# Optimization experiments

Measured on AMD Instinct MI355X. Metric: run time of the kernel, lower is better.

## Reference

```python
import jax, jax.numpy as jnp
import numpy as np

B, T, E, H, D = 2, 2048, 1024, 16, 64   # batch, seq, n_embd, heads, head_dim
C, P, BF, MH, R, F4 = 64, 64, 256, 128, 8, 4096  # ctx_dim, prototypes, basis, mod hidden, gate rank, 4*n_embd


def _rms(x):
    return x * jax.lax.rsqrt(jnp.mean(x * x, axis=-1, keepdims=True) + 1e-6)


def _rotary(x, cos, sin):
    d = x.shape[-1] // 2
    x1, x2 = x[..., :d], x[..., d:]
    return jnp.concatenate([x1 * cos + x2 * sin, -x1 * sin + x2 * cos], axis=-1)


def _ln(x, g, b):
    mu = jnp.mean(x, axis=-1, keepdims=True)
    v = jnp.mean(jnp.square(x - mu), axis=-1, keepdims=True)
    return (x - mu) * jax.lax.rsqrt(v + 1e-5) * g + b


def _remixed(x, ctx, bw, lg, lb, tm, bias, m1w, m1b, m2w, m2b, ogw, ogb, ogB, ogs):
    # RemixedLinear: basis proj -> LayerNorm -> context sigmoid gate -> template mixing -> low-rank output gate
    h = _ln(x @ bw.T, lg, lb)                                              # [B,T,basis]
    gl = jax.nn.gelu(ctx @ m1w.T + m1b, approximate=False) @ m2w.T + m2b   # basis_modulator MLP
    gate_basis = jax.nn.sigmoid(gl)                                        # gate_temperature = 1.0, dense gate
    gate_out = 1.0 + jnp.tanh(ogs * ((ctx @ ogw.T + ogb) @ ogB))           # low-rank output gate
    return (h * gate_basis) @ tm.T * gate_out + bias


def _forward(x, cos, sin, wq, wk, wv, wo, cb_qw, protos,
             fc_bw, fc_lg, fc_lb, fc_tm, fc_b, fc_m1w, fc_m1b, fc_m2w, fc_m2b, fc_ogw, fc_ogb, fc_ogB, fc_ogs,
             pj_bw, pj_lg, pj_lb, pj_tm, pj_b, pj_m1w, pj_m1b, pj_m2w, pj_m2b, pj_ogw, pj_ogb, pj_ogB, pj_ogs):
    b, t, _ = x.shape
    # --- attention with rotary embeddings ---
    xn = _rms(x)
    q = _rotary((xn @ wq.T).reshape(b, t, H, D), cos, sin)
    k = _rotary((xn @ wk.T).reshape(b, t, H, D), cos, sin)
    v = (xn @ wv.T).reshape(b, t, H, D)
    s = jnp.einsum('bqhd,bkhd->bhqk', q, k) * (D ** -0.5)
    mask = jnp.tril(jnp.ones((t, t), dtype=bool))
    s = jnp.where(mask, s, jnp.finfo(s.dtype).min)
    a = jax.nn.softmax(s, axis=-1)
    attn_out = jnp.einsum('bhqk,bkhd->bqhd', a, v).reshape(b, t, E) @ wo.T
    x = x + attn_out
    # --- ContextBank: soft lookup into prototype vocabulary ---
    xn2 = _rms(x)
    cq = xn2 @ cb_qw.T                                  # [B,T,C]
    w = jax.nn.softmax((cq @ protos.T) * (C ** -0.5), axis=-1)
    ctx = w @ protos                                    # [B,T,C]
    # --- RemixedFeedForward: RemixedLinear -> relu^2 -> RemixedLinear ---
    h = _remixed(xn2, ctx, fc_bw, fc_lg, fc_lb, fc_tm, fc_b, fc_m1w, fc_m1b, fc_m2w, fc_m2b, fc_ogw, fc_ogb, fc_ogB, fc_ogs)
    h = jnp.square(jax.nn.relu(h))
    y = _remixed(h, ctx, pj_bw, pj_lg, pj_lb, pj_tm, pj_b, pj_m1w, pj_m1b, pj_m2w, pj_m2b, pj_ogw, pj_ogb, pj_ogB, pj_ogs)
    return x + y


def setup_inputs():
    key = jax.random.key(0)
    ks = jax.random.split(key, 24)
    g = lambda i, shape, s=0.02: jax.random.normal(ks[i], shape, jnp.float32) * s
    t = jnp.arange(T, dtype=jnp.float32)
    inv = 1.0 / (10000.0 ** (jnp.arange(0, D, 2, dtype=jnp.float32) / D))
    ang = t[:, None] * inv                              # [T, D/2]
    return dict(
        x=jax.random.normal(ks[0], (B, T, E), jnp.float32),
        cos=jnp.cos(ang)[None, :, None, :], sin=jnp.sin(ang)[None, :, None, :],
        wq=g(1, (E, E)), wk=g(2, (E, E)), wv=g(3, (E, E)), wo=g(4, (E, E)),
        cb_qw=g(5, (C, E)), protos=g(6, (P, C)),
        fc_bw=g(7, (BF, E)), fc_lg=jnp.ones((BF,)), fc_lb=jnp.zeros((BF,)),
        fc_tm=g(8, (F4, BF), 0.05), fc_b=jnp.zeros((F4,)),
        fc_m1w=g(9, (MH, C)), fc_m1b=jnp.zeros((MH,)),
        fc_m2w=g(10, (BF, MH)), fc_m2b=jnp.zeros((BF,)),
        fc_ogw=g(11, (R, C)), fc_ogb=jnp.zeros((R,)),
        fc_ogB=g(12, (R, F4)), fc_ogs=jnp.full((1,), 0.1, jnp.float32),
        pj_bw=g(13, (BF, F4)), pj_lg=jnp.ones((BF,)), pj_lb=jnp.zeros((BF,)),
        pj_tm=g(14, (E, BF), 0.05), pj_b=jnp.zeros((E,)),
        pj_m1w=g(15, (MH, C)), pj_m1b=jnp.zeros((MH,)),
        pj_m2w=g(16, (BF, MH)), pj_m2b=jnp.zeros((BF,)),
        pj_ogw=g(17, (R, C)), pj_ogb=jnp.zeros((R,)),
        pj_ogB=g(18, (R, E)), pj_ogs=jnp.full((1,), 0.1, jnp.float32),
    )


def reference(x, cos, sin, wq, wk, wv, wo, cb_qw, protos,
              fc_bw, fc_lg, fc_lb, fc_tm, fc_b, fc_m1w, fc_m1b, fc_m2w, fc_m2b, fc_ogw, fc_ogb, fc_ogB, fc_ogs,
              pj_bw, pj_lg, pj_lb, pj_tm, pj_b, pj_m1w, pj_m1b, pj_m2w, pj_m2b, pj_ogw, pj_ogb, pj_ogB, pj_ogs):
    return _forward(x, cos, sin, wq, wk, wv, wo, cb_qw, protos,
                    fc_bw, fc_lg, fc_lb, fc_tm, fc_b, fc_m1w, fc_m1b, fc_m2w, fc_m2b, fc_ogw, fc_ogb, fc_ogB, fc_ogs,
                    pj_bw, pj_lg, pj_lb, pj_tm, pj_b, pj_m1w, pj_m1b, pj_m2w, pj_m2b, pj_ogw, pj_ogb, pj_ogB, pj_ogs)
```

## Files before the change

### kernel.cpp

```cpp
#include <hip/hip_runtime.h>
#include <hip/hip_bf16.h>

typedef unsigned short u16;
typedef unsigned int u32;
typedef __attribute__((ext_vector_type(8))) short bf16x8;
typedef __attribute__((ext_vector_type(4))) float f32x4;
typedef __attribute__((ext_vector_type(4))) u16 u16x4;

#define DEVFN __device__ __forceinline__

DEVFN u16 f2b(float f) {
  u32 u = __builtin_bit_cast(u32, f);
  return (u16)((u + 0x7FFFu + ((u >> 16) & 1u)) >> 16);
}
DEVFN float b2f(u16 b) { return __builtin_bit_cast(float, (u32)b << 16); }

DEVFN void gll16(const void* g, void* l) {
  __builtin_amdgcn_global_load_lds((const __attribute__((address_space(1))) void*)g,
                                   (__attribute__((address_space(3))) void*)l, 16, 0, 0);
}
#define BARRIER() __builtin_amdgcn_s_barrier()

constexpr int Tc = 2048, Ec = 1024, Hc = 16, Cc = 64, BFc = 256, F4c = 4096;
constexpr int Mc = 2 * Tc;

constexpr size_t MB = 1ull << 20;
constexpr size_t O_XN  = 0;
constexpr size_t O_HBF = 8 * MB;
constexpr size_t O_QB  = 40 * MB;
constexpr size_t O_H1  = 40 * MB;
constexpr size_t O_A2  = 40 * MB;
constexpr size_t O_KB  = 48 * MB;
constexpr size_t O_H2  = 48 * MB;
constexpr size_t O_VBF = 56 * MB;
constexpr size_t O_CQ  = 64 * MB;
constexpr size_t O_CTX = 68 * MB;
constexpr size_t O_GO1 = 68 * MB + 512 * 1024;
constexpr size_t O_GO2 = 68 * MB + 640 * 1024;
constexpr size_t O_GB1 = 69 * MB;
constexpr size_t O_VT  = 72 * MB;
constexpr size_t O_GB2 = 73 * MB;
constexpr size_t O_A1  = 77 * MB;
constexpr size_t O_X2  = 80 * MB;
constexpr size_t O_WQ  = 96 * MB, O_WK = 98 * MB, O_WV = 100 * MB, O_WO = 102 * MB;
constexpr size_t O_CBQ = 104 * MB;
constexpr size_t O_FCBW = O_CBQ + 256 * 1024;
constexpr size_t O_FCTM = 105 * MB;
constexpr size_t O_PJBW = 107 * MB;
constexpr size_t O_PJTM = 109 * MB;

struct Cvt9 {
  const float* s[9];
  u16* d[9];
  int cum[10];
};
__global__ __launch_bounds__(256) void k_cvt(Cvt9 a) {
  int i = blockIdx.x * 256 + threadIdx.x;
  int seg = 0;
  #pragma unroll
  for (int s = 1; s < 9; s++) seg += (i >= a.cum[s]);
  int off = i - a.cum[seg];
  float4 v = *(const float4*)&a.s[seg][(size_t)off * 4];
  u16x4 o; o.x = f2b(v.x); o.y = f2b(v.y); o.z = f2b(v.z); o.w = f2b(v.w);
  *(u16x4*)&a.d[seg][(size_t)off * 4] = o;
}

DEVFN float bsum256(float v, float* sb) {
  #pragma unroll
  for (int off = 32; off; off >>= 1) v += __shfl_down(v, off);
  __syncthreads();
  if ((threadIdx.x & 63) == 0) sb[threadIdx.x >> 6] = v;
  __syncthreads();
  return (sb[0] + sb[1]) + (sb[2] + sb[3]);
}

__global__ __launch_bounds__(256) void k_rms(const float* __restrict__ x, u16* __restrict__ o) {
  __shared__ float sb[4];
  int row = blockIdx.x, tid = threadIdx.x;
  float4 v = *(const float4*)&x[(size_t)row * 1024 + tid * 4];
  float s = bsum256(v.x * v.x + v.y * v.y + v.z * v.z + v.w * v.w, sb);
  float r = rsqrtf(s * (1.f / 1024.f) + 1e-6f);
  u16x4 ov;
  ov.x = f2b(v.x * r); ov.y = f2b(v.y * r); ov.z = f2b(v.z * r); ov.w = f2b(v.w * r);
  *(u16x4*)&o[(size_t)row * 1024 + tid * 4] = ov;
}

__global__ __launch_bounds__(256) void k_vtrans(const u16* __restrict__ vb, u16* __restrict__ vt) {
  __shared__ u16 tl[64][65];
  int t0 = blockIdx.x * 64, bh = blockIdx.y;
  int b = bh >> 4, h = bh & 15, tid = threadIdx.x;
  #pragma unroll
  for (int rep = 0; rep < 16; rep++) {
    int idx = rep * 256 + tid, r = idx >> 6, c = idx & 63;
    tl[r][c] = vb[((size_t)(b * 2048 + t0 + r)) * 1024 + h * 64 + c];
  }
  __syncthreads();
  #pragma unroll
  for (int rep = 0; rep < 16; rep++) {
    int idx = rep * 256 + tid, d = idx >> 6, tt = idx & 63;
    vt[((size_t)bh * 64 + d) * 2048 + t0 + tt] = tl[tt][d];
  }
}

#define MFMA16(A, B, C) __builtin_amdgcn_mfma_f32_16x16x32_bf16(A, B, C, 0, 0, 0)
__global__ __launch_bounds__(256) void k_attn(const u16* __restrict__ Q, const u16* __restrict__ Kb,
                                              const u16* __restrict__ VT, u16* __restrict__ O) {
  const int h = blockIdx.y, b = blockIdx.z;
  const int tid = threadIdx.x, lane = tid & 63, w = tid >> 6;
  const int lr = lane & 15, lg = lane >> 4;
  const size_t TE = 2048ull * 1024ull;
  const u16* Qp = Q + (size_t)b * TE + (size_t)h * 64;
  const u16* Kp = Kb + (size_t)b * TE + (size_t)h * 64;
  const u16* Vp = VT + ((size_t)(b * 16 + h)) * 64ull * 2048ull;
  u16* Op = O + (size_t)b * TE + (size_t)h * 64;
  __shared__ __align__(16) u16 Ks[2][4096];
  __shared__ __align__(16) u16 Vs[2][4096];
  __shared__ __align__(16) u16 Ps[4][1024];
  auto stageKV = [&](int j0, int buf) {
    #pragma unroll
    for (int c = 0; c < 2; c++) {
      int u = c * 256 + tid;
      int row = u >> 3, slot = u & 7;
      int cg = slot ^ (row & 7);
      gll16(&Kp[(size_t)(j0 + row) * 1024 + cg * 8], &Ks[buf][u * 8]);
    }
    #pragma unroll
    for (int c = 0; c < 2; c++) {
      int u = c * 256 + tid;
      int row = u >> 3, slot = u & 7;
      int cg = slot ^ (row & 7);
      gll16(&Vp[(size_t)row * 2048 + j0 + cg * 8], &Vs[buf][u * 8]);
    }
  };
  auto run_tile = [&](int qb) {
    const int q0 = qb * 64, qw0 = q0 + w * 16;
    bf16x8 qf0 = *(const bf16x8*)&Qp[(size_t)(qw0 + lr) * 1024 + lg * 8];
    bf16x8 qf1 = *(const bf16x8*)&Qp[(size_t)(qw0 + lr) * 1024 + 32 + lg * 8];
    f32x4 o0 = {}, o1 = {}, o2 = {}, o3 = {};
    float m = -1e30f, l = 0.f;
    const int NT = qb + 1;
    stageKV(0, 0);
    int cur = 0;
    for (int it = 0; it < NT; it++) {
      if (it + 1 < NT) {
        stageKV((it + 1) * 64, cur ^ 1);
        asm volatile("s_waitcnt vmcnt(4)" ::: "memory");
      } else {
        asm volatile("s_waitcnt vmcnt(0)" ::: "memory");
      }
      BARRIER();
      const int j0 = it * 64;
      const u16* Kl = Ks[cur];
      const u16* Vl = Vs[cur];
      f32x4 c4[4];
      __builtin_amdgcn_s_setprio(1);
      #pragma unroll
      for (int kg = 0; kg < 4; kg++) {
        f32x4 cc = {};
        int r = kg * 16 + lr;
        bf16x8 ka0 = *(const bf16x8*)&Kl[r * 64 + ((lg ^ (lr & 7)) * 8)];
        bf16x8 ka1 = *(const bf16x8*)&Kl[r * 64 + (((4 + lg) ^ (lr & 7)) * 8)];
        cc = MFMA16(ka0, qf0, cc);
        cc = MFMA16(ka1, qf1, cc);
        c4[kg] = cc;
      }
      __builtin_amdgcn_s_setprio(0);
      float xs[16];
      #pragma unroll
      for (int kg = 0; kg < 4; kg++)
        #pragma unroll
        for (int r = 0; r < 4; r++) xs[kg * 4 + r] = c4[kg][r] * 0.125f;
      if (it == NT - 1) {
        int q = qw0 + lr;
        #pragma unroll
        for (int kg = 0; kg < 4; kg++)
          #pragma unroll
          for (int r = 0; r < 4; r++)
            if (j0 + kg * 16 + lg * 4 + r > q) xs[kg * 4 + r] = -1e30f;
      }
      float tm = xs[0];
      #pragma unroll
      for (int r = 1; r < 16; r++) tm = fmaxf(tm, xs[r]);
      tm = fmaxf(tm, __shfl_xor(tm, 16));
      tm = fmaxf(tm, __shfl_xor(tm, 32));
      float mn = fmaxf(m, tm);
      float al = __expf(m - mn);
      m = mn;
      float p[16], rs = 0.f;
      #pragma unroll
      for (int r = 0; r < 16; r++) { p[r] = __expf(xs[r] - mn); rs += p[r]; }
      rs += __shfl_xor(rs, 16);
      rs += __shfl_xor(rs, 32);
      l = l * al + rs;
      #pragma unroll
      for (int kg = 0; kg < 4; kg++) {
        int unit = (kg >> 1) * 64 + ((kg & 1) * 2 + (lg >> 1)) * 16 + lr;
        u16x4 pk;
        pk.x = f2b(p[kg * 4 + 0]); pk.y = f2b(p[kg * 4 + 1]);
        pk.z = f2b(p[kg * 4 + 2]); pk.w = f2b(p[kg * 4 + 3]);
        *(u16x4*)&Ps[w][unit * 8 + (lg & 1) * 4] = pk;
      }
      float ar0 = __shfl(al, lg * 4 + 0), ar1 = __shfl(al, lg * 4 + 1);
      float ar2 = __shfl(al, lg * 4 + 2), ar3 = __shfl(al, lg * 4 + 3);
      o0[0] *= ar0; o0[1] *= ar1; o0[2] *= ar2; o0[3] *= ar3;
      o1[0] *= ar0; o1[1] *= ar1; o1[2] *= ar2; o1[3] *= ar3;
      o2[0] *= ar0; o2[1] *= ar1; o2[2] *= ar2; o2[3] *= ar3;
      o3[0] *= ar0; o3[1] *= ar1; o3[2] *= ar2; o3[3] *= ar3;
      bf16x8 pa0 = *(const bf16x8*)&Ps[w][(lg * 16 + lr) * 8];
      bf16x8 pa1 = *(const bf16x8*)&Ps[w][(64 + lg * 16 + lr) * 8];
      __builtin_amdgcn_s_setprio(1);
      #pragma unroll
      for (int dg = 0; dg < 4; dg++) {
        int dr = dg * 16 + lr;
        bf16x8 v0 = *(const bf16x8*)&Vl[dr * 64 + ((lg ^ (lr & 7)) * 8)];
        bf16x8 v1 = *(const bf16x8*)&Vl[dr * 64 + (((4 + lg) ^ (lr & 7)) * 8)];
        f32x4& od = (dg == 0) ? o0 : (dg == 1) ? o1 : (dg == 2) ? o2 : o3;
        od = MFMA16(pa0, v0, od);
        od = MFMA16(pa1, v1, od);
      }
      __builtin_amdgcn_s_setprio(0);
      BARRIER();
      cur ^= 1;
    }
    float li0 = 1.f / __shfl(l, lg * 4 + 0), li1 = 1.f / __shfl(l, lg * 4 + 1);
    float li2 = 1.f / __shfl(l, lg * 4 + 2), li3 = 1.f / __shfl(l, lg * 4 + 3);
    #pragma unroll
    for (int r = 0; r < 4; r++) {
      float lir = (r == 0) ? li0 : (r == 1) ? li1 : (r == 2) ? li2 : li3;
      size_t ro = (size_t)(qw0 + lg * 4 + r) * 1024;
      Op[ro + lr]      = f2b(o0[r] * lir);
      Op[ro + 16 + lr] = f2b(o1[r] * lir);
      Op[ro + 32 + lr] = f2b(o2[r] * lir);
      Op[ro + 48 + lr] = f2b(o3[r] * lir);
    }
  };
  run_tile(blockIdx.x);
  run_tile(31 - blockIdx.x);
}

template <int BM, int BN, int WR, int WC, int EPI>
__global__ __launch_bounds__(256) void gemm_bt(
    const u16* __restrict__ A, const u16* __restrict__ Bw,
    float* __restrict__ Co, u16* __restrict__ Cb,
    int gM, int N, int K, int KS,
    const float* __restrict__ e0, const float* __restrict__ e1,
    const float* __restrict__ e2, const float* __restrict__ e3,
    const float* __restrict__ e4) {
  constexpr int WM = BM / WR, WN = BN / WC;
  constexpr int FM = WM / 16, FN = WN / 16;
  constexpr int ACH = BM / 64, BCH = BN / 64;
  static_assert(WR * WC == 4 && BM % 64 == 0 && BN % 64 == 0, "cfg");
  __shared__ __align__(16) u16 As[2][BM * 32];
  __shared__ __align__(16) u16 Bs[2][BN * 32];
  const int tid = threadIdx.x;
  const int lane = tid & 63, wid = tid >> 6;
  const int wr = wid / WC, wc = wid % WC;
  const int bm = blockIdx.y * BM, bn = blockIdx.x * BN;
  const int lr = lane & 15, lg = lane >> 4;
  const int arow0 = bm + wr * WM, bcol0 = bn + wc * WN;
  const int kbeg = blockIdx.z * KS, kend = kbeg + KS;
  f32x4 acc[FM][FN] = {};
  auto stage = [&](int k0, int buf) {
    #pragma unroll
    for (int c = 0; c < ACH; c++) {
      int u = c * 256 + tid;
      int row = u >> 2, slot = u & 3;
      int cg = slot ^ (row & 3) ^ ((row >> 2) & 3);
      gll16(&A[(size_t)(bm + row) * K + k0 + cg * 8], &As[buf][u * 8]);
    }
    #pragma unroll
    for (int c = 0; c < BCH; c++) {
      int u = c * 256 + tid;
      int row = u >> 2, slot = u & 3;
      int cg = slot ^ (row & 3) ^ ((row >> 2) & 3);
      gll16(&Bw[(size_t)(bn + row) * K + k0 + cg * 8], &Bs[buf][u * 8]);
    }
  };
  stage(kbeg, 0);
  int cur = 0;
  for (int k0 = kbeg; k0 < kend; k0 += 32) {
    __syncthreads();
    if (k0 + 32 < kend) stage(k0 + 32, cur ^ 1);
    const u16* Ab = As[cur];
    const u16* Bb = Bs[cur];
    bf16x8 af[FM], bfr[FN];
    #pragma unroll
    for (int i = 0; i < FM; i++) {
      int tr = wr * WM + i * 16 + lr;
      af[i] = *(const bf16x8*)&Ab[tr * 32 + ((lg ^ (tr & 3) ^ ((tr >> 2) & 3)) * 8)];
    }
    #pragma unroll
    for (int j = 0; j < FN; j++) {
      int tr = wc * WN + j * 16 + lr;
      bfr[j] = *(const bf16x8*)&Bb[tr * 32 + ((lg ^ (tr & 3) ^ ((tr >> 2) & 3)) * 8)];
    }
    #pragma unroll
    for (int i = 0; i < FM; i++)
      #pragma unroll
      for (int j = 0; j < FN; j++)
        acc[i][j] = __builtin_amdgcn_mfma_f32_16x16x32_bf16(af[i], bfr[j], acc[i][j], 0, 0, 0);
    cur ^= 1;
  }
  const int nb0 = bcol0 + lr;
  if constexpr (EPI == 0 || EPI == 2) {
    float* Cz = Co + (size_t)blockIdx.z * ((size_t)gM * N);
    #pragma unroll
    for (int i = 0; i < FM; i++)
      #pragma unroll
      for (int r = 0; r < 4; r++) {
        size_t mrow = (size_t)(arow0 + i * 16 + lg * 4 + r);
        #pragma unroll
        for (int j = 0; j < FN; j++) {
          float v = acc[i][j][r];
          if constexpr (EPI == 2) v += e4[mrow * N + nb0 + j * 16];
          Cz[mrow * N + nb0 + j * 16] = v;
        }
      }
  } else if constexpr (EPI == 5) {
    #pragma unroll
    for (int i = 0; i < FM; i++)
      #pragma unroll
      for (int r = 0; r < 4; r++) {
        size_t mrow = (size_t)(arow0 + i * 16 + lg * 4 + r);
        int t = (int)(mrow & 2047);
        #pragma unroll
        for (int j = 0; j < 2; j++) {
          int d = lr + j * 16;
          float cth = e0[t * 32 + d], sth = e1[t * 32 + d];
          float x1 = acc[i][j][r], x2 = acc[i][j + 2][r];
          Cb[mrow * N + nb0 + j * 16]       = f2b(x1 * cth + x2 * sth);
          Cb[mrow * N + nb0 + (j + 2) * 16] = f2b(x2 * cth - x1 * sth);
        }
      }
  } else if constexpr (EPI == 7) {
    #pragma unroll
    for (int i = 0; i < FM; i++)
      #pragma unroll
      for (int r = 0; r < 4; r++) {
        size_t mrow = (size_t)(arow0 + i * 16 + lg * 4 + r);
        #pragma unroll
        for (int j = 0; j < FN; j++)
          Cb[mrow * N + nb0 + j * 16] = f2b(acc[i][j][r]);
      }
  } else {
    const float ogs = e3[0];
    float gB[FN][8], bias[FN];
    #pragma unroll
    for (int j = 0; j < FN; j++) {
      int n = nb0 + j * 16;
      bias[j] = e2[n];
      #pragma unroll
      for (int rr = 0; rr < 8; rr++) gB[j][rr] = e1[(size_t)rr * N + n];
    }
    #pragma unroll
    for (int i = 0; i < FM; i++)
      #pragma unroll
      for (int r = 0; r < 4; r++) {
        size_t mrow = (size_t)(arow0 + i * 16 + lg * 4 + r);
        float go8[8];
        #pragma unroll
        for (int rr = 0; rr < 8; rr++) go8[rr] = e0[mrow * 8 + rr];
        #pragma unroll
        for (int j = 0; j < FN; j++) {
          float d = 0.f;
          #pragma unroll
          for (int rr = 0; rr < 8; rr++) d += go8[rr] * gB[j][rr];
          float gate = 1.f + tanhf(ogs * d);
          float v = acc[i][j][r] * gate + bias[j];
          if constexpr (EPI == 3) {
            v = fmaxf(v, 0.f); v *= v;
            Cb[mrow * N + nb0 + j * 16] = f2b(v);
          } else {
            v += e4[mrow * N + nb0 + j * 16];
            Co[mrow * N + nb0 + j * 16] = v;
          }
        }
      }
  }
}

__global__ __launch_bounds__(256) void k_ctx(const float* __restrict__ cqp,
                                             const float* __restrict__ pr,
                                             u16* __restrict__ ctx) {
  __shared__ float pl[64 * 65];
  __shared__ float cqs[4][64];
  __shared__ float wl[4][64];
  int tid = threadIdx.x, lane = tid & 63, w = tid >> 6;
  int row0 = blockIdx.x * 4;
  for (int i = w; i < 64; i += 4) pl[i * 65 + lane] = pr[i * 64 + lane];
  {
    float s4 = 0.f;
    #pragma unroll
    for (int z = 0; z < 4; z++) s4 += cqp[(size_t)z * Mc * 64 + (size_t)(row0 + w) * 64 + lane];
    cqs[w][lane] = s4;
  }
  __syncthreads();
  float s = 0.f;
  #pragma unroll
  for (int k = 0; k < 64; k++) s += cqs[w][k] * pl[lane * 65 + k];
  s *= 0.125f;
  float mx = s;
  #pragma unroll
  for (int off = 32; off; off >>= 1) mx = fmaxf(mx, __shfl_xor(mx, off));
  float e = __expf(s - mx), sum = e;
  #pragma unroll
  for (int off = 32; off; off >>= 1) sum += __shfl_xor(sum, off);
  wl[w][lane] = e / sum;
  __syncthreads();
  float a = 0.f;
  #pragma unroll
  for (int p = 0; p < 64; p++) a += wl[w][p] * pl[p * 65 + lane];
  ctx[(size_t)(row0 + w) * 64 + lane] = f2b(a);
}

__global__ __launch_bounds__(256) void k_gate(
    const u16* __restrict__ ctx,
    const float* __restrict__ m1w, const float* __restrict__ m1b,
    const float* __restrict__ m2w, const float* __restrict__ m2b,
    const float* __restrict__ ogw, const float* __restrict__ ogb,
    float* __restrict__ gb, float* __restrict__ go) {
  __shared__ __align__(16) float cs[16][64];
  __shared__ __align__(16) float gls[16][128];
  int tid = threadIdx.x;
  int row0 = blockIdx.x * 16;
  for (int i = tid; i < 16 * 64; i += 256) cs[i >> 6][i & 63] = b2f(ctx[(size_t)row0 * 64 + i]);
  __syncthreads();
  for (int i = tid; i < 16 * 128; i += 256) {
    int r = i >> 7, mh = i & 127;
    const float* wrow = &m1w[(size_t)mh * 64];
    float a = m1b[mh];
    #pragma unroll
    for (int k4 = 0; k4 < 16; k4++) {
      float4 w4 = *(const float4*)&wrow[k4 * 4];
      float4 c4 = *(const float4*)&cs[r][k4 * 4];
      a += c4.x * w4.x + c4.y * w4.y + c4.z * w4.z + c4.w * w4.w;
    }
    gls[r][mh] = 0.5f * a * (1.f + erff(a * 0.70710678f));
  }
  if (tid < 128) {
    int r = tid >> 3, rr = tid & 7;
    const float* wrow = &ogw[(size_t)rr * 64];
    float a = ogb[rr];
    #pragma unroll
    for (int k4 = 0; k4 < 16; k4++) {
      float4 w4 = *(const float4*)&wrow[k4 * 4];
      float4 c4 = *(const float4*)&cs[r][k4 * 4];
      a += c4.x * w4.x + c4.y * w4.y + c4.z * w4.z + c4.w * w4.w;
    }
    go[(size_t)(row0 + r) * 8 + rr] = a;
  }
  __syncthreads();
  int n = tid;
  float acc[16];
  #pragma unroll
  for (int r = 0; r < 16; r++) acc[r] = m2b[n];
  for (int k4 = 0; k4 < 32; k4++) {
    float4 wv = *(const float4*)&m2w[(size_t)n * 128 + k4 * 4];
    #pragma unroll
    for (int r = 0; r < 16; r++) {
      float4 g = *(const float4*)&gls[r][k4 * 4];
      acc[r] += g.x * wv.x + g.y * wv.y + g.z * wv.z + g.w * wv.w;
    }
  }
  #pragma unroll
  for (int r = 0; r < 16; r++)
    gb[(size_t)(row0 + r) * 256 + n] = 1.f / (1.f + __expf(-acc[r]));
}

template <int NS>
__global__ __launch_bounds__(256) void k_lnmul(const float* __restrict__ h,
                                               const float* __restrict__ g,
                                               const float* __restrict__ b,
                                               const float* __restrict__ gbm,
                                               u16* __restrict__ o) {
  __shared__ float sb[4];
  int row = blockIdx.x, n = threadIdx.x;
  float x = 0.f;
  #pragma unroll
  for (int z = 0; z < NS; z++) x += h[(size_t)z * Mc * 256 + (size_t)row * 256 + n];
  float mu = bsum256(x, sb) * (1.f / 256.f);
  float d = x - mu;
  float var = bsum256(d * d, sb) * (1.f / 256.f);
  float y = d * rsqrtf(var + 1e-5f) * g[n] + b[n];
  o[(size_t)row * 256 + n] = f2b(y * gbm[(size_t)row * 256 + n]);
}

extern "C" void kernel_launch(void* const* d_in, const int* in_sizes, int n_in,
                              void* d_out, int out_size, void* d_ws, size_t ws_size,
                              hipStream_t stream) {
  (void)in_sizes; (void)n_in; (void)out_size; (void)ws_size;
  const float* x      = (const float*)d_in[0];
  const float* cosb   = (const float*)d_in[1];
  const float* sinb   = (const float*)d_in[2];
  const float* wq     = (const float*)d_in[3];
  const float* wk     = (const float*)d_in[4];
  const float* wv     = (const float*)d_in[5];
  const float* wo     = (const float*)d_in[6];
  const float* cb_qw  = (const float*)d_in[7];
  const float* protos = (const float*)d_in[8];
  const float* fc_bw  = (const float*)d_in[9];
  const float* fc_lg  = (const float*)d_in[10];
  const float* fc_lb  = (const float*)d_in[11];
  const float* fc_tm  = (const float*)d_in[12];
  const float* fc_b   = (const float*)d_in[13];
  const float* fc_m1w = (const float*)d_in[14];
  const float* fc_m1b = (const float*)d_in[15];
  const float* fc_m2w = (const float*)d_in[16];
  const float* fc_m2b = (const float*)d_in[17];
  const float* fc_ogw = (const float*)d_in[18];
  const float* fc_ogb = (const float*)d_in[19];
  const float* fc_ogB = (const float*)d_in[20];
  const float* fc_ogs = (const float*)d_in[21];
  const float* pj_bw  = (const float*)d_in[22];
  const float* pj_lg  = (const float*)d_in[23];
  const float* pj_lb  = (const float*)d_in[24];
  const float* pj_tm  = (const float*)d_in[25];
  const float* pj_b   = (const float*)d_in[26];
  const float* pj_m1w = (const float*)d_in[27];
  const float* pj_m1b = (const float*)d_in[28];
  const float* pj_m2w = (const float*)d_in[29];
  const float* pj_m2b = (const float*)d_in[30];
  const float* pj_ogw = (const float*)d_in[31];
  const float* pj_ogb = (const float*)d_in[32];
  const float* pj_ogB = (const float*)d_in[33];
  const float* pj_ogs = (const float*)d_in[34];
  char* ws = (char*)d_ws;
  float* outp = (float*)d_out;
  auto U = [&](size_t o) { return (u16*)(ws + o); };
  auto F = [&](size_t o) { return (float*)(ws + o); };
  const float* nf = nullptr;

  {
    Cvt9 a;
    const float* srcs[9] = {wq, wk, wv, wo, cb_qw, fc_bw, fc_tm, pj_bw, pj_tm};
    size_t offs[9] = {O_WQ, O_WK, O_WV, O_WO, O_CBQ, O_FCBW, O_FCTM, O_PJBW, O_PJTM};
    int ns[9] = {Ec*Ec, Ec*Ec, Ec*Ec, Ec*Ec, Cc*Ec, BFc*Ec, F4c*BFc, BFc*F4c, Ec*BFc};
    int cum = 0;
    for (int s = 0; s < 9; s++) {
      a.s[s] = srcs[s]; a.d[s] = U(offs[s]); a.cum[s] = cum; cum += ns[s] / 4;
    }
    a.cum[9] = cum;
    k_cvt<<<dim3(cum / 256), dim3(256), 0, stream>>>(a);
  }
  k_rms<<<dim3(Mc), dim3(256), 0, stream>>>(x, U(O_XN));
  gemm_bt<128,128,2,2,5><<<dim3(8,32), dim3(256), 0, stream>>>(U(O_XN), U(O_WQ), nullptr, U(O_QB), Mc, Ec, Ec, Ec, cosb, sinb, nf, nf, nf);
  gemm_bt<128,128,2,2,5><<<dim3(8,32), dim3(256), 0, stream>>>(U(O_XN), U(O_WK), nullptr, U(O_KB), Mc, Ec, Ec, Ec, cosb, sinb, nf, nf, nf);
  gemm_bt<128,128,2,2,7><<<dim3(8,32), dim3(256), 0, stream>>>(U(O_XN), U(O_WV), nullptr, U(O_VBF), Mc, Ec, Ec, Ec, nf, nf, nf, nf, nf);
  k_vtrans<<<dim3(Tc / 64, 2 * Hc), dim3(256), 0, stream>>>(U(O_VBF), U(O_VT));
  k_attn<<<dim3(Tc / 128, Hc, 2), dim3(256), 0, stream>>>(U(O_QB), U(O_KB), U(O_VT), U(O_XN));
  gemm_bt<128,128,2,2,2><<<dim3(8,32), dim3(256), 0, stream>>>(U(O_XN), U(O_WO), F(O_X2), nullptr, Mc, Ec, Ec, Ec, nf, nf, nf, nf, x);
  k_rms<<<dim3(Mc), dim3(256), 0, stream>>>(F(O_X2), U(O_XN));
  gemm_bt<64,64,1,4,0><<<dim3(1,64,4), dim3(256), 0, stream>>>(U(O_XN), U(O_CBQ), F(O_CQ), nullptr, Mc, Cc, Ec, 256, nf, nf, nf, nf, nf);
  k_ctx<<<dim3(Mc / 4), dim3(256), 0, stream>>>(F(O_CQ), protos, U(O_CTX));
  k_gate<<<dim3(Mc / 16), dim3(256), 0, stream>>>(U(O_CTX), fc_m1w, fc_m1b, fc_m2w, fc_m2b, fc_ogw, fc_ogb, F(O_GB1), F(O_GO1));
  k_gate<<<dim3(Mc / 16), dim3(256), 0, stream>>>(U(O_CTX), pj_m1w, pj_m1b, pj_m2w, pj_m2b, pj_ogw, pj_ogb, F(O_GB2), F(O_GO2));
  gemm_bt<64,64,1,4,0><<<dim3(4,64,2), dim3(256), 0, stream>>>(U(O_XN), U(O_FCBW), F(O_H1), nullptr, Mc, BFc, Ec, 512, nf, nf, nf, nf, nf);
  k_lnmul<2><<<dim3(Mc), dim3(256), 0, stream>>>(F(O_H1), fc_lg, fc_lb, F(O_GB1), U(O_A1));
  gemm_bt<128,128,2,2,3><<<dim3(32,32), dim3(256), 0, stream>>>(U(O_A1), U(O_FCTM), nullptr, U(O_HBF), Mc, F4c, BFc, BFc, F(O_GO1), fc_ogB, fc_b, fc_ogs, nf);
  gemm_bt<64,64,1,4,0><<<dim3(4,64,4), dim3(256), 0, stream>>>(U(O_HBF), U(O_PJBW), F(O_H2), nullptr, Mc, BFc, F4c, 1024, nf, nf, nf, nf, nf);
  k_lnmul<4><<<dim3(Mc), dim3(256), 0, stream>>>(F(O_H2), pj_lg, pj_lb, F(O_GB2), U(O_A2));
  gemm_bt<128,128,2,2,4><<<dim3(8,32), dim3(256), 0, stream>>>(U(O_A2), U(O_PJTM), outp, nullptr, Mc, Ec, BFc, BFc, F(O_GO2), pj_ogB, pj_b, pj_ogs, F(O_X2));
}
```

Baseline: 487.0 us.

## Fuse QKV GEMMs, merge context and gate kernels, lazy softmax rescale, retile GEMMs

The Q, K and V projections become one GEMM with N=3072 whose epilogue routes tiles to Q/K (with rotary) or V buffers. The context lookup and both gate MLPs are merged into one kernel, which removes the bf16 ctx round trip and two launches. Attention now uses exp2 with a folded scale, rescales the running output only when the row max grows by more than a threshold, and remaps its blocks into a 1D grid. Several GEMMs switch to 128x64 tiles. The lazy rescale adds a warp vote and relies on the bounded-growth assumption staying numerically safe.

```diff
diff --git a/kernel.cpp b/kernel.cpp
--- a/kernel.cpp
+++ b/kernel.cpp
@@ -23,6 +23,7 @@
 
 constexpr int Tc = 2048, Ec = 1024, Hc = 16, Cc = 64, BFc = 256, F4c = 4096;
 constexpr int Mc = 2 * Tc;
+constexpr float C8 = 0.18033688f;
 
 constexpr size_t MB = 1ull << 20;
 constexpr size_t O_XN  = 0;
@@ -34,7 +35,6 @@
 constexpr size_t O_H2  = 48 * MB;
 constexpr size_t O_VBF = 56 * MB;
 constexpr size_t O_CQ  = 64 * MB;
-constexpr size_t O_CTX = 68 * MB;
 constexpr size_t O_GO1 = 68 * MB + 512 * 1024;
 constexpr size_t O_GO2 = 68 * MB + 640 * 1024;
 constexpr size_t O_GB1 = 69 * MB;
@@ -105,7 +105,10 @@
 #define MFMA16(A, B, C) __builtin_amdgcn_mfma_f32_16x16x32_bf16(A, B, C, 0, 0, 0)
 __global__ __launch_bounds__(256) void k_attn(const u16* __restrict__ Q, const u16* __restrict__ Kb,
                                               const u16* __restrict__ VT, u16* __restrict__ O) {
-  const int h = blockIdx.y, b = blockIdx.z;
+  const int i = blockIdx.x;
+  const int wrk = (i & 7) * 64 + (i >> 3);
+  const int hb = wrk >> 4, xp = wrk & 15;
+  const int b = hb >> 4, h = hb & 15;
   const int tid = threadIdx.x, lane = tid & 63, w = tid >> 6;
   const int lr = lane & 15, lg = lane >> 4;
   const size_t TE = 2048ull * 1024ull;
@@ -169,7 +172,7 @@
       #pragma unroll
       for (int kg = 0; kg < 4; kg++)
         #pragma unroll
-        for (int r = 0; r < 4; r++) xs[kg * 4 + r] = c4[kg][r] * 0.125f;
+        for (int r = 0; r < 4; r++) xs[kg * 4 + r] = c4[kg][r];
       if (it == NT - 1) {
         int q = qw0 + lr;
         #pragma unroll
@@ -183,15 +186,25 @@
       for (int r = 1; r < 16; r++) tm = fmaxf(tm, xs[r]);
       tm = fmaxf(tm, __shfl_xor(tm, 16));
       tm = fmaxf(tm, __shfl_xor(tm, 32));
-      float mn = fmaxf(m, tm);
-      float al = __expf(m - mn);
-      m = mn;
+      if (!__all(tm <= m + 64.f)) {
+        float mn = fmaxf(m, tm);
+        float al = exp2f((m - mn) * C8);
+        m = mn;
+        l *= al;
+        float ar0 = __shfl(al, lg * 4 + 0), ar1 = __shfl(al, lg * 4 + 1);
+        float ar2 = __shfl(al, lg * 4 + 2), ar3 = __shfl(al, lg * 4 + 3);
+        o0[0] *= ar0; o0[1] *= ar1; o0[2] *= ar2; o0[3] *= ar3;
+        o1[0] *= ar0; o1[1] *= ar1; o1[2] *= ar2; o1[3] *= ar3;
+        o2[0] *= ar0; o2[1] *= ar1; o2[2] *= ar2; o2[3] *= ar3;
+        o3[0] *= ar0; o3[1] *= ar1; o3[2] *= ar2; o3[3] *= ar3;
+      }
+      const float mnC = -m * C8;
       float p[16], rs = 0.f;
       #pragma unroll
-      for (int r = 0; r < 16; r++) { p[r] = __expf(xs[r] - mn); rs += p[r]; }
+      for (int r = 0; r < 16; r++) { p[r] = exp2f(fmaf(xs[r], C8, mnC)); rs += p[r]; }
       rs += __shfl_xor(rs, 16);
       rs += __shfl_xor(rs, 32);
-      l = l * al + rs;
+      l += rs;
       #pragma unroll
       for (int kg = 0; kg < 4; kg++) {
         int unit = (kg >> 1) * 64 + ((kg & 1) * 2 + (lg >> 1)) * 16 + lr;
@@ -200,12 +213,6 @@
         pk.z = f2b(p[kg * 4 + 2]); pk.w = f2b(p[kg * 4 + 3]);
         *(u16x4*)&Ps[w][unit * 8 + (lg & 1) * 4] = pk;
       }
-      float ar0 = __shfl(al, lg * 4 + 0), ar1 = __shfl(al, lg * 4 + 1);
-      float ar2 = __shfl(al, lg * 4 + 2), ar3 = __shfl(al, lg * 4 + 3);
-      o0[0] *= ar0; o0[1] *= ar1; o0[2] *= ar2; o0[3] *= ar3;
-      o1[0] *= ar0; o1[1] *= ar1; o1[2] *= ar2; o1[3] *= ar3;
-      o2[0] *= ar0; o2[1] *= ar1; o2[2] *= ar2; o2[3] *= ar3;
-      o3[0] *= ar0; o3[1] *= ar1; o3[2] *= ar2; o3[3] *= ar3;
       bf16x8 pa0 = *(const bf16x8*)&Ps[w][(lg * 16 + lr) * 8];
       bf16x8 pa1 = *(const bf16x8*)&Ps[w][(64 + lg * 16 + lr) * 8];
       __builtin_amdgcn_s_setprio(1);
@@ -234,14 +241,14 @@
       Op[ro + 48 + lr] = f2b(o3[r] * lir);
     }
   };
-  run_tile(blockIdx.x);
-  run_tile(31 - blockIdx.x);
+  run_tile(xp);
+  run_tile(31 - xp);
 }
 
 template <int BM, int BN, int WR, int WC, int EPI>
 __global__ __launch_bounds__(256) void gemm_bt(
     const u16* __restrict__ A, const u16* __restrict__ Bw,
-    float* __restrict__ Co, u16* __restrict__ Cb,
+    float* __restrict__ Co, u16* __restrict__ Cb, u16* __restrict__ Cb2, u16* __restrict__ Cb3,
     int gM, int N, int K, int KS,
     const float* __restrict__ e0, const float* __restrict__ e1,
     const float* __restrict__ e2, const float* __restrict__ e3,
@@ -316,22 +323,37 @@
           Cz[mrow * N + nb0 + j * 16] = v;
         }
       }
-  } else if constexpr (EPI == 5) {
-    #pragma unroll
-    for (int i = 0; i < FM; i++)
-      #pragma unroll
-      for (int r = 0; r < 4; r++) {
-        size_t mrow = (size_t)(arow0 + i * 16 + lg * 4 + r);
-        int t = (int)(mrow & 2047);
-        #pragma unroll
-        for (int j = 0; j < 2; j++) {
-          int d = lr + j * 16;
-          float cth = e0[t * 32 + d], sth = e1[t * 32 + d];
-          float x1 = acc[i][j][r], x2 = acc[i][j + 2][r];
-          Cb[mrow * N + nb0 + j * 16]       = f2b(x1 * cth + x2 * sth);
-          Cb[mrow * N + nb0 + (j + 2) * 16] = f2b(x2 * cth - x1 * sth);
+  } else if constexpr (EPI == 8) {
+    if (bn < 2048) {
+      u16* dst = (bn < 1024) ? Cb : Cb2;
+      const int nq0 = (bcol0 & 1023) + lr;
+      #pragma unroll
+      for (int i = 0; i < FM; i++)
+        #pragma unroll
+        for (int r = 0; r < 4; r++) {
+          size_t mrow = (size_t)(arow0 + i * 16 + lg * 4 + r);
+          int t = (int)(mrow & 2047);
+          #pragma unroll
+          for (int j = 0; j < 2; j++) {
+            int d = lr + j * 16;
+            float cth = e0[t * 32 + d], sth = e1[t * 32 + d];
+            float x1 = acc[i][j][r], x2 = acc[i][j + 2][r];
+            dst[mrow * 1024 + nq0 + j * 16]       = f2b(x1 * cth + x2 * sth);
+            dst[mrow * 1024 + nq0 + (j + 2) * 16] = f2b(x2 * cth - x1 * sth);
+          }
         }
-      }
+    } else {
+      const int nv0 = (bcol0 - 2048) + lr;
+      #pragma unroll
+      for (int i = 0; i < FM; i++)
+        #pragma unroll
+        for (int r = 0; r < 4; r++) {
+          size_t mrow = (size_t)(arow0 + i * 16 + lg * 4 + r);
+          #pragma unroll
+          for (int j = 0; j < FN; j++)
+            Cb3[mrow * 1024 + nv0 + j * 16] = f2b(acc[i][j][r]);
+        }
+    }
   } else if constexpr (EPI == 7) {
     #pragma unroll
     for (int i = 0; i < FM; i++)
@@ -379,92 +401,112 @@
   }
 }
 
-__global__ __launch_bounds__(256) void k_ctx(const float* __restrict__ cqp,
-                                             const float* __restrict__ pr,
-                                             u16* __restrict__ ctx) {
+__global__ __launch_bounds__(256) void k_ctxgate(
+    const float* __restrict__ cqp, const float* __restrict__ pr,
+    const float* __restrict__ f_m1w, const float* __restrict__ f_m1b,
+    const float* __restrict__ f_m2w, const float* __restrict__ f_m2b,
+    const float* __restrict__ f_ogw, const float* __restrict__ f_ogb,
+    const float* __restrict__ p_m1w, const float* __restrict__ p_m1b,
+    const float* __restrict__ p_m2w, const float* __restrict__ p_m2b,
+    const float* __restrict__ p_ogw, const float* __restrict__ p_ogb,
+    float* __restrict__ gb1, float* __restrict__ go1,
+    float* __restrict__ gb2, float* __restrict__ go2) {
   __shared__ float pl[64 * 65];
-  __shared__ float cqs[4][64];
-  __shared__ float wl[4][64];
-  int tid = threadIdx.x, lane = tid & 63, w = tid >> 6;
-  int row0 = blockIdx.x * 4;
-  for (int i = w; i < 64; i += 4) pl[i * 65 + lane] = pr[i * 64 + lane];
-  {
-    float s4 = 0.f;
-    #pragma unroll
-    for (int z = 0; z < 4; z++) s4 += cqp[(size_t)z * Mc * 64 + (size_t)(row0 + w) * 64 + lane];
-    cqs[w][lane] = s4;
-  }
-  __syncthreads();
-  float s = 0.f;
-  #pragma unroll
-  for (int k = 0; k < 64; k++) s += cqs[w][k] * pl[lane * 65 + k];
-  s *= 0.125f;
-  float mx = s;
-  #pragma unroll
-  for (int off = 32; off; off >>= 1) mx = fmaxf(mx, __shfl_xor(mx, off));
-  float e = __expf(s - mx), sum = e;
-  #pragma unroll
-  for (int off = 32; off; off >>= 1) sum += __shfl_xor(sum, off);
-  wl[w][lane] = e / sum;
-  __syncthreads();
-  float a = 0.f;
-  #pragma unroll
-  for (int p = 0; p < 64; p++) a += wl[w][p] * pl[p * 65 + lane];
-  ctx[(size_t)(row0 + w) * 64 + lane] = f2b(a);
-}
-
-__global__ __launch_bounds__(256) void k_gate(
-    const u16* __restrict__ ctx,
-    const float* __restrict__ m1w, const float* __restrict__ m1b,
-    const float* __restrict__ m2w, const float* __restrict__ m2b,
-    const float* __restrict__ ogw, const float* __restrict__ ogb,
-    float* __restrict__ gb, float* __restrict__ go) {
+  __shared__ __align__(16) float cqs[16][64];
+  __shared__ float wl[16][64];
   __shared__ __align__(16) float cs[16][64];
   __shared__ __align__(16) float gls[16][128];
-  int tid = threadIdx.x;
-  int row0 = blockIdx.x * 16;
-  for (int i = tid; i < 16 * 64; i += 256) cs[i >> 6][i & 63] = b2f(ctx[(size_t)row0 * 64 + i]);
+  const int tid = threadIdx.x;
+  const int row0 = blockIdx.x * 16;
+  for (int idx = tid; idx < 4096; idx += 256) pl[(idx >> 6) * 65 + (idx & 63)] = pr[idx];
+  for (int idx = tid; idx < 1024; idx += 256) {
+    int r = idx >> 6, c = idx & 63;
+    float s = 0.f;
+    #pragma unroll
+    for (int z = 0; z < 4; z++) s += cqp[(size_t)z * Mc * 64 + (size_t)(row0 + r) * 64 + c];
+    cqs[r][c] = s;
+  }
   __syncthreads();
-  for (int i = tid; i < 16 * 128; i += 256) {
-    int r = i >> 7, mh = i & 127;
-    const float* wrow = &m1w[(size_t)mh * 64];
-    float a = m1b[mh];
+  const int row = tid >> 4, pg = tid & 15;
+  float sc[4];
+  #pragma unroll
+  for (int q = 0; q < 4; q++) {
+    int p = pg * 4 + q;
+    float s = 0.f;
     #pragma unroll
     for (int k4 = 0; k4 < 16; k4++) {
-      float4 w4 = *(const float4*)&wrow[k4 * 4];
-      float4 c4 = *(const float4*)&cs[r][k4 * 4];
-      a += c4.x * w4.x + c4.y * w4.y + c4.z * w4.z + c4.w * w4.w;
-    }
-    gls[r][mh] = 0.5f * a * (1.f + erff(a * 0.70710678f));
-  }
-  if (tid < 128) {
-    int r = tid >> 3, rr = tid & 7;
-    const float* wrow = &ogw[(size_t)rr * 64];
-    float a = ogb[rr];
-    #pragma unroll
-    for (int k4 = 0; k4 < 16; k4++) {
-      float4 w4 = *(const float4*)&wrow[k4 * 4];
-      float4 c4 = *(const float4*)&cs[r][k4 * 4];
-      a += c4.x * w4.x + c4.y * w4.y + c4.z * w4.z + c4.w * w4.w;
-    }
-    go[(size_t)(row0 + r) * 8 + rr] = a;
-  }
+      float4 cv = *(const float4*)&cqs[row][k4 * 4];
+      const float* pw = &pl[p * 65 + k4 * 4];
+      s += cv.x * pw[0] + cv.y * pw[1] + cv.z * pw[2] + cv.w * pw[3];
+    }
+    sc[q] = s * 0.125f;
+  }
+  float mx = fmaxf(fmaxf(sc[0], sc[1]), fmaxf(sc[2], sc[3]));
+  #pragma unroll
+  for (int off = 1; off <= 8; off <<= 1) mx = fmaxf(mx, __shfl_xor(mx, off));
+  float e[4], sum = 0.f;
+  #pragma unroll
+  for (int q = 0; q < 4; q++) { e[q] = __expf(sc[q] - mx); sum += e[q]; }
+  #pragma unroll
+  for (int off = 1; off <= 8; off <<= 1) sum += __shfl_xor(sum, off);
+  float inv = 1.f / sum;
+  #pragma unroll
+  for (int q = 0; q < 4; q++) wl[row][pg * 4 + q] = e[q] * inv;
   __syncthreads();
-  int n = tid;
-  float acc[16];
-  #pragma unroll
-  for (int r = 0; r < 16; r++) acc[r] = m2b[n];
-  for (int k4 = 0; k4 < 32; k4++) {
-    float4 wv = *(const float4*)&m2w[(size_t)n * 128 + k4 * 4];
-    #pragma unroll
-    for (int r = 0; r < 16; r++) {
-      float4 g = *(const float4*)&gls[r][k4 * 4];
-      acc[r] += g.x * wv.x + g.y * wv.y + g.z * wv.z + g.w * wv.w;
-    }
-  }
-  #pragma unroll
-  for (int r = 0; r < 16; r++)
-    gb[(size_t)(row0 + r) * 256 + n] = 1.f / (1.f + __expf(-acc[r]));
+  #pragma unroll
+  for (int q = 0; q < 4; q++) {
+    int c = pg * 4 + q;
+    float a = 0.f;
+    for (int p = 0; p < 64; p++) a += wl[row][p] * pl[p * 65 + c];
+    cs[row][c] = a;
+  }
+  __syncthreads();
+  auto gate = [&](const float* m1w, const float* m1b, const float* m2w, const float* m2b,
+                  const float* ogw, const float* ogb, float* gb, float* go) {
+    for (int idx = tid; idx < 2048; idx += 256) {
+      int r = idx >> 7, mh = idx & 127;
+      const float* wrow = &m1w[(size_t)mh * 64];
+      float a = m1b[mh];
+      #pragma unroll
+      for (int k4 = 0; k4 < 16; k4++) {
+        float4 w4 = *(const float4*)&wrow[k4 * 4];
+        float4 c4v = *(const float4*)&cs[r][k4 * 4];
+        a += c4v.x * w4.x + c4v.y * w4.y + c4v.z * w4.z + c4v.w * w4.w;
+      }
+      gls[r][mh] = 0.5f * a * (1.f + erff(a * 0.70710678f));
+    }
+    if (tid < 128) {
+      int r = tid >> 3, rr = tid & 7;
+      const float* wrow = &ogw[(size_t)rr * 64];
+      float a = ogb[rr];
+      #pragma unroll
+      for (int k4 = 0; k4 < 16; k4++) {
+        float4 w4 = *(const float4*)&wrow[k4 * 4];
+        float4 c4v = *(const float4*)&cs[r][k4 * 4];
+        a += c4v.x * w4.x + c4v.y * w4.y + c4v.z * w4.z + c4v.w * w4.w;
+      }
+      go[(size_t)(row0 + r) * 8 + rr] = a;
+    }
+    __syncthreads();
+    int n = tid;
+    float acc2[16];
+    #pragma unroll
+    for (int r = 0; r < 16; r++) acc2[r] = m2b[n];
+    for (int k4 = 0; k4 < 32; k4++) {
+      float4 wv = *(const float4*)&m2w[(size_t)n * 128 + k4 * 4];
+      #pragma unroll
+      for (int r = 0; r < 16; r++) {
+        float4 g = *(const float4*)&gls[r][k4 * 4];
+        acc2[r] += g.x * wv.x + g.y * wv.y + g.z * wv.z + g.w * wv.w;
+      }
+    }
+    #pragma unroll
+    for (int r = 0; r < 16; r++)
+      gb[(size_t)(row0 + r) * 256 + n] = 1.f / (1.f + __expf(-acc2[r]));
+    __syncthreads();
+  };
+  gate(f_m1w, f_m1b, f_m2w, f_m2b, f_ogw, f_ogb, gb1, go1);
+  gate(p_m1w, p_m1b, p_m2w, p_m2b, p_ogw, p_ogb, gb2, go2);
 }
 
 template <int NS>
@@ -529,6 +571,7 @@
   auto U = [&](size_t o) { return (u16*)(ws + o); };
   auto F = [&](size_t o) { return (float*)(ws + o); };
   const float* nf = nullptr;
+  u16* nu = nullptr;
 
   {
     Cvt9 a;
@@ -543,21 +586,20 @@
     k_cvt<<<dim3(cum / 256), dim3(256), 0, stream>>>(a);
   }
   k_rms<<<dim3(Mc), dim3(256), 0, stream>>>(x, U(O_XN));
-  gemm_bt<128,128,2,2,5><<<dim3(8,32), dim3(256), 0, stream>>>(U(O_XN), U(O_WQ), nullptr, U(O_QB), Mc, Ec, Ec, Ec, cosb, sinb, nf, nf, nf);
-  gemm_bt<128,128,2,2,5><<<dim3(8,32), dim3(256), 0, stream>>>(U(O_XN), U(O_WK), nullptr, U(O_KB), Mc, Ec, Ec, Ec, cosb, sinb, nf, nf, nf);
-  gemm_bt<128,128,2,2,7><<<dim3(8,32), dim3(256), 0, stream>>>(U(O_XN), U(O_WV), nullptr, U(O_VBF), Mc, Ec, Ec, Ec, nf, nf, nf, nf, nf);
+  gemm_bt<128,128,2,2,8><<<dim3(24,32), dim3(256), 0, stream>>>(U(O_XN), U(O_WQ), nullptr, U(O_QB), U(O_KB), U(O_VBF), Mc, 3072, Ec, Ec, cosb, sinb, nf, nf, nf);
   k_vtrans<<<dim3(Tc / 64, 2 * Hc), dim3(256), 0, stream>>>(U(O_VBF), U(O_VT));
-  k_attn<<<dim3(Tc / 128, Hc, 2), dim3(256), 0, stream>>>(U(O_QB), U(O_KB), U(O_VT), U(O_XN));
-  gemm_bt<128,128,2,2,2><<<dim3(8,32), dim3(256), 0, stream>>>(U(O_XN), U(O_WO), F(O_X2), nullptr, Mc, Ec, Ec, Ec, nf, nf, nf, nf, x);
+  k_attn<<<dim3(512), dim3(256), 0, stream>>>(U(O_QB), U(O_KB), U(O_VT), U(O_XN));
+  gemm_bt<128,64,2,2,2><<<dim3(16,32), dim3(256), 0, stream>>>(U(O_XN), U(O_WO), F(O_X2), nu, nu, nu, Mc, Ec, Ec, Ec, nf, nf, nf, nf, x);
   k_rms<<<dim3(Mc), dim3(256), 0, stream>>>(F(O_X2), U(O_XN));
-  gemm_bt<64,64,1,4,0><<<dim3(1,64,4), dim3(256), 0, stream>>>(U(O_XN), U(O_CBQ), F(O_CQ), nullptr, Mc, Cc, Ec, 256, nf, nf, nf, nf, nf);
-  k_ctx<<<dim3(Mc / 4), dim3(256), 0, stream>>>(F(O_CQ), protos, U(O_CTX));
-  k_gate<<<dim3(Mc / 16), dim3(256), 0, stream>>>(U(O_CTX), fc_m1w, fc_m1b, fc_m2w, fc_m2b, fc_ogw, fc_ogb, F(O_GB1), F(O_GO1));
-  k_gate<<<dim3(Mc / 16), dim3(256), 0, stream>>>(U(O_CTX), pj_m1w, pj_m1b, pj_m2w, pj_m2b, pj_ogw, pj_ogb, F(O_GB2), F(O_GO2));
-  gemm_bt<64,64,1,4,0><<<dim3(4,64,2), dim3(256), 0, stream>>>(U(O_XN), U(O_FCBW), F(O_H1), nullptr, Mc, BFc, Ec, 512, nf, nf, nf, nf, nf);
+  gemm_bt<64,64,1,4,0><<<dim3(1,64,4), dim3(256), 0, stream>>>(U(O_XN), U(O_CBQ), F(O_CQ), nu, nu, nu, Mc, Cc, Ec, 256, nf, nf, nf, nf, nf);
+  k_ctxgate<<<dim3(Mc / 16), dim3(256), 0, stream>>>(F(O_CQ), protos,
+      fc_m1w, fc_m1b, fc_m2w, fc_m2b, fc_ogw, fc_ogb,
+      pj_m1w, pj_m1b, pj_m2w, pj_m2b, pj_ogw, pj_ogb,
+      F(O_GB1), F(O_GO1), F(O_GB2), F(O_GO2));
+  gemm_bt<64,64,1,4,0><<<dim3(4,64,2), dim3(256), 0, stream>>>(U(O_XN), U(O_FCBW), F(O_H1), nu, nu, nu, Mc, BFc, Ec, 512, nf, nf, nf, nf, nf);
   k_lnmul<2><<<dim3(Mc), dim3(256), 0, stream>>>(F(O_H1), fc_lg, fc_lb, F(O_GB1), U(O_A1));
-  gemm_bt<128,128,2,2,3><<<dim3(32,32), dim3(256), 0, stream>>>(U(O_A1), U(O_FCTM), nullptr, U(O_HBF), Mc, F4c, BFc, BFc, F(O_GO1), fc_ogB, fc_b, fc_ogs, nf);
-  gemm_bt<64,64,1,4,0><<<dim3(4,64,4), dim3(256), 0, stream>>>(U(O_HBF), U(O_PJBW), F(O_H2), nullptr, Mc, BFc, F4c, 1024, nf, nf, nf, nf, nf);
+  gemm_bt<128,128,2,2,3><<<dim3(32,32), dim3(256), 0, stream>>>(U(O_A1), U(O_FCTM), nullptr, U(O_HBF), nu, nu, Mc, F4c, BFc, BFc, F(O_GO1), fc_ogB, fc_b, fc_ogs, nf);
+  gemm_bt<128,64,2,2,0><<<dim3(4,32,4), dim3(256), 0, stream>>>(U(O_HBF), U(O_PJBW), F(O_H2), nu, nu, nu, Mc, BFc, F4c, 1024, nf, nf, nf, nf, nf);
   k_lnmul<4><<<dim3(Mc), dim3(256), 0, stream>>>(F(O_H2), pj_lg, pj_lb, F(O_GB2), U(O_A2));
-  gemm_bt<128,128,2,2,4><<<dim3(8,32), dim3(256), 0, stream>>>(U(O_A2), U(O_PJTM), outp, nullptr, Mc, Ec, BFc, BFc, F(O_GO2), pj_ogB, pj_b, pj_ogs, F(O_X2));
-}
+  gemm_bt<128,64,2,2,4><<<dim3(16,32), dim3(256), 0, stream>>>(U(O_A2), U(O_PJTM), outp, nu, nu, nu, Mc, Ec, BFc, BFc, F(O_GO2), pj_ogB, pj_b, pj_ogs, F(O_X2));
+}
```

Measured after the change: 544.2 us. 1.12x slower.
